# Kernel tuning notes

Hardware: AMD Instinct MI355X
Metric: run time of the kernel (lower is better)

Reference implementation:

```python
import jax, jax.numpy as jnp
import numpy as np

B, PLEN, QLEN, D = 16, 1024, 256, 256
MASK_VALUE = -10000000.0


def setup_inputs() -> dict:
    key = jax.random.key(0)
    k1, k2, k3 = jax.random.split(key, 3)
    passage = jax.random.normal(k1, (B, PLEN, D), dtype=jnp.float32)
    question = jax.random.normal(k2, (B, QLEN, D), dtype=jnp.float32)
    passage_mask = (jnp.arange(PLEN)[None, :] >= int(PLEN * 0.9)).astype(jnp.int32)
    passage_mask = jnp.broadcast_to(passage_mask, (B, PLEN))
    question_mask = (jnp.arange(QLEN)[None, :] >= int(QLEN * 0.9)).astype(jnp.int32)
    question_mask = jnp.broadcast_to(question_mask, (B, QLEN))
    # score_linear: Linear(3d, 1) -> weight vector [3d], scalar bias
    W = jax.random.normal(k3, (3 * D,), dtype=jnp.float32) * 0.05
    b = jnp.zeros((1,), dtype=jnp.float32)
    return {"passage": passage, "question": question,
            "passage_mask": passage_mask, "question_mask": question_mask,
            "W": W, "b": b}


def reference(passage, question, passage_mask, question_mask, W, b):
    d = passage.shape[-1]
    # Decompose Linear([p, q, p*q]) @ W + b into three additive terms --
    # identical math to concat+linear, no [b,plen,qlen,3d] intermediate.
    w_p, w_q, w_pq = W[:d], W[d:2 * d], W[2 * d:]
    score = (jnp.einsum('bpd,d->bp', passage, w_p)[:, :, None]
             + jnp.einsum('bqd,d->bq', question, w_q)[:, None, :]
             + jnp.einsum('bpd,bqd->bpq', passage * w_pq, question)
             + b[0])  # [b, plen, qlen]
    pm = passage_mask.astype(score.dtype)
    qm = question_mask.astype(score.dtype)
    keep = (1.0 - pm)[:, :, None] * (1.0 - qm)[:, None, :]  # [b,plen,qlen]
    mask = 1.0 - keep
    score = score * keep + mask * MASK_VALUE
    p2q_weights = jax.nn.softmax(score, axis=2)
    q2p_weights = jax.nn.softmax(jnp.transpose(score, (0, 2, 1)), axis=2)
    p2q_weights = p2q_weights * keep
    q2p_weights = q2p_weights * jnp.transpose(keep, (0, 2, 1))
    p2q_attention = jnp.einsum('bpq,bqd->bpd', p2q_weights, question)
    q2p_attention = jnp.einsum('bqp,bpd->bqd', q2p_weights, passage)
    coattention = jnp.einsum('bpq,bqd->bpd', p2q_weights, q2p_attention)
    return (p2q_attention, coattention)
```

## Files before the change

### kernel.cpp

```cpp
#include <hip/hip_runtime.h>
#include <math.h>

#define NB 16
#define PLEN 1024
#define QLEN 256
#define DIM 256
#define MASKV -10000000.0f

typedef __attribute__((ext_vector_type(8))) short short8;
typedef __attribute__((ext_vector_type(4))) float f32x4;

union u4x16 { unsigned short u[4]; int2 v; };
union u8x16 { unsigned short u[8]; int4 v; };
union u16x16 { unsigned short u[16]; int4 v[2]; };

__device__ inline unsigned short f2bf(float x) {
  unsigned int u = __float_as_uint(x);
  u += 0x7FFF + ((u >> 16) & 1);
  return (unsigned short)(u >> 16);
}
__device__ inline float bf2f(unsigned short u) {
  return __uint_as_float(((unsigned int)u) << 16);
}
__device__ inline int4 pack8(float4 a, float4 b) {
  u8x16 o;
  o.u[0] = f2bf(a.x); o.u[1] = f2bf(a.y); o.u[2] = f2bf(a.z); o.u[3] = f2bf(a.w);
  o.u[4] = f2bf(b.x); o.u[5] = f2bf(b.y); o.u[6] = f2bf(b.z); o.u[7] = f2bf(b.w);
  return o.v;
}

__global__ __launch_bounds__(1024) void k_scoreA(
    const float* __restrict__ passage, const float* __restrict__ question,
    const float* __restrict__ Wg,
    const int* __restrict__ pmask, const int* __restrict__ qmask,
    const float* __restrict__ bias,
    unsigned short* __restrict__ PbT, unsigned short* __restrict__ QbT,
    float* __restrict__ CM, float* __restrict__ CL,
    float* __restrict__ RM, float* __restrict__ RL,
    unsigned short* __restrict__ P2Q, unsigned short* __restrict__ P2Qt) {
  int bid0 = blockIdx.x;
  int bid = (bid0 & 7) * 32 + (bid0 >> 3);
  int b = bid >> 4;
  int tile = bid & 15;
  int p0 = tile * 64;
  int t = threadIdx.x, lane = t & 63, wv = t >> 6;
  int s = wv >> 2, h = wv & 3;
  __shared__ __align__(16) unsigned short As[2][64][40];
  __shared__ __align__(16) unsigned short Bs[2][256][40];
  __shared__ __align__(16) unsigned short Pl[64][264];
  __shared__ float redM[4][256], redL[4][256];
  __shared__ float rowM[64][4], rowL[64][4];
  __shared__ float spS[64];
  __shared__ float sqS[256];

  int rb = t >> 2, cb = (t & 3) * 8;
  int pr = t >> 4, pc = (t & 15) * 2;
  const float* psrc = passage + ((size_t)b * PLEN + p0 + pr) * DIM;
  const float* qsrc = question + ((size_t)b * QLEN + rb) * DIM;
  const float* wq = Wg + DIM;

  f32x4 acc[4] = {};
  float spp = 0.f, sqq = 0.f;
  float4 qa = *(const float4*)&qsrc[cb];
  float4 qb_ = *(const float4*)&qsrc[cb + 4];
  float2 xv = *(const float2*)(psrc + pc);
  {
    sqq += qa.x * wq[cb]     + qa.y * wq[cb + 1] + qa.z * wq[cb + 2] + qa.w * wq[cb + 3]
         + qb_.x * wq[cb + 4] + qb_.y * wq[cb + 5] + qb_.z * wq[cb + 6] + qb_.w * wq[cb + 7];
    *(int4*)&Bs[0][rb][cb] = pack8(qa, qb_);
    spp += xv.x * Wg[pc] + xv.y * Wg[pc + 1];
    unsigned int raw = (unsigned int)f2bf(xv.x) | (((unsigned int)f2bf(xv.y)) << 16);
    unsigned int wgt = (unsigned int)f2bf(xv.x * Wg[2 * DIM + pc])
                     | (((unsigned int)f2bf(xv.y * Wg[2 * DIM + pc + 1])) << 16);
    *(unsigned int*)&Pl[pr][pc] = raw;
    *(unsigned int*)&As[0][pr][pc] = wgt;
  }
  __syncthreads();
  int cur = 0;
  for (int ki = 0; ki < 8; ++ki) {
    float2 xn; float4 qa2, qb2;
    if (ki < 7) {
      int kt = (ki + 1) * 32;
      qa2 = *(const float4*)&qsrc[kt + cb];
      qb2 = *(const float4*)&qsrc[kt + cb + 4];
      xn = *(const float2*)(psrc + kt + pc);
    }
    short8 af = *(const short8*)&As[cur][s * 16 + (lane & 15)][(lane >> 4) * 8];
    for (int j = 0; j < 4; ++j) {
      short8 bf = *(const short8*)&Bs[cur][h * 64 + j * 16 + (lane & 15)][(lane >> 4) * 8];
      acc[j] = __builtin_amdgcn_mfma_f32_16x16x32_bf16(af, bf, acc[j], 0, 0, 0);
    }
    if (ki < 7) {
      int kt = (ki + 1) * 32;
      int dq = kt + cb, dp = kt + pc;
      sqq += qa2.x * wq[dq]     + qa2.y * wq[dq + 1] + qa2.z * wq[dq + 2] + qa2.w * wq[dq + 3]
           + qb2.x * wq[dq + 4] + qb2.y * wq[dq + 5] + qb2.z * wq[dq + 6] + qb2.w * wq[dq + 7];
      spp += xn.x * Wg[dp] + xn.y * Wg[dp + 1];
      unsigned int raw = (unsigned int)f2bf(xn.x) | (((unsigned int)f2bf(xn.y)) << 16);
      unsigned int wgt = (unsigned int)f2bf(xn.x * Wg[2 * DIM + dp])
                       | (((unsigned int)f2bf(xn.y * Wg[2 * DIM + dp + 1])) << 16);
      int nxt = cur ^ 1;
      *(unsigned int*)&Pl[pr][dp] = raw;
      *(unsigned int*)&As[nxt][pr][pc] = wgt;
      *(int4*)&Bs[nxt][rb][cb] = pack8(qa2, qb2);
      cur = nxt;
    }
    __syncthreads();
  }

  sqq += __shfl_xor(sqq, 1, 64);
  sqq += __shfl_xor(sqq, 2, 64);
  if ((t & 3) == 0) sqS[rb] = sqq;
  spp += __shfl_xor(spp, 1, 64);
  spp += __shfl_xor(spp, 2, 64);
  spp += __shfl_xor(spp, 4, 64);
  spp += __shfl_xor(spp, 8, 64);
  if ((t & 15) == 0) spS[pr] = spp;
  {
    int d = t >> 2, ch = t & 3;
    u16x16 o;
    for (int e = 0; e < 16; ++e) o.u[e] = Pl[ch * 16 + e][d];
    unsigned short* dst = PbT + ((size_t)b * DIM + d) * PLEN + p0 + ch * 16;
    *(int4*)dst = o.v[0];
    *(int4*)(dst + 8) = o.v[1];
  }
  __syncthreads();

  float b0 = bias[0];
  int prow[4]; float spv[4]; int pmv[4];
  for (int r = 0; r < 4; ++r) {
    int rl = s * 16 + (lane >> 4) * 4 + r;
    prow[r] = p0 + rl;
    spv[r] = spS[rl] + b0;
    pmv[r] = pmask[b * PLEN + prow[r]];
  }
  float sqv[4]; int qmv[4];
  for (int j = 0; j < 4; ++j) {
    int q = h * 64 + j * 16 + (lane & 15);
    sqv[j] = sqS[q];
    qmv[j] = qmask[b * QLEN + q];
  }
  for (int j = 0; j < 4; ++j)
    for (int r = 0; r < 4; ++r) {
      float v = acc[j][r] + spv[r] + sqv[j];
      if (pmv[r] | qmv[j]) v = MASKV;
      acc[j][r] = v;
    }

  for (int j = 0; j < 4; ++j) {
    float m = fmaxf(fmaxf(acc[j][0], acc[j][1]), fmaxf(acc[j][2], acc[j][3]));
    m = fmaxf(m, __shfl_xor(m, 16, 64));
    m = fmaxf(m, __shfl_xor(m, 32, 64));
    float e = 0.f;
    for (int r = 0; r < 4; ++r) e += __expf(acc[j][r] - m);
    e += __shfl_xor(e, 16, 64);
    e += __shfl_xor(e, 32, 64);
    if ((lane >> 4) == 0) {
      redM[s][h * 64 + j * 16 + (lane & 15)] = m;
      redL[s][h * 64 + j * 16 + (lane & 15)] = e;
    }
  }
  for (int r = 0; r < 4; ++r) {
    int rl = s * 16 + (lane >> 4) * 4 + r;
    float m = acc[0][r];
    for (int j = 1; j < 4; ++j) m = fmaxf(m, acc[j][r]);
    for (int msk = 1; msk <= 8; msk <<= 1) m = fmaxf(m, __shfl_xor(m, msk, 64));
    float l = 0.f;
    for (int j = 0; j < 4; ++j) l += __expf(acc[j][r] - m);
    for (int msk = 1; msk <= 8; msk <<= 1) l += __shfl_xor(l, msk, 64);
    if ((lane & 15) == 0) { rowM[rl][h] = m; rowL[rl][h] = l; }
  }
  __syncthreads();

  if (t < 256) {
    int q = t;
    float M = fmaxf(fmaxf(redM[0][q], redM[1][q]), fmaxf(redM[2][q], redM[3][q]));
    float L = redL[0][q] * __expf(redM[0][q] - M) + redL[1][q] * __expf(redM[1][q] - M)
            + redL[2][q] * __expf(redM[2][q] - M) + redL[3][q] * __expf(redM[3][q] - M);
    size_t o = ((size_t)b * 16 + tile) * QLEN + q;
    CM[o] = M; CL[o] = L;
  }

  for (int r = 0; r < 4; ++r) {
    int rl = s * 16 + (lane >> 4) * 4 + r;
    float m0 = rowM[rl][0], m1 = rowM[rl][1], m2 = rowM[rl][2], m3 = rowM[rl][3];
    float m = fmaxf(fmaxf(m0, m1), fmaxf(m2, m3));
    float l = rowL[rl][0] * __expf(m0 - m) + rowL[rl][1] * __expf(m1 - m)
            + rowL[rl][2] * __expf(m2 - m) + rowL[rl][3] * __expf(m3 - m);
    if (h == 0 && (lane & 15) == 0) {
      RM[(size_t)b * PLEN + p0 + rl] = m;
      RL[(size_t)b * PLEN + p0 + rl] = l;
    }
    float inv = 1.0f / l;
    for (int j = 0; j < 4; ++j) {
      float e = (pmv[r] | qmv[j]) ? 0.0f : __expf(acc[j][r] - m) * inv;
      Pl[rl][h * 64 + j * 16 + (lane & 15)] = f2bf(e);
    }
  }
  __syncthreads();

  for (int k = 0; k < 2; ++k) {
    int idx = t + k * 1024;
    int row = idx >> 5, c8 = idx & 31;
    *(int4*)&P2Q[((size_t)b * PLEN + p0 + row) * QLEN + c8 * 8] = *(const int4*)&Pl[row][c8 * 8];
  }
  {
    int q = t >> 2, pcc = t & 3;
    u16x16 o;
    for (int e = 0; e < 16; ++e) o.u[e] = Pl[pcc * 16 + e][q];
    unsigned short* dst = P2Qt + ((size_t)b * QLEN + q) * PLEN + p0 + pcc * 16;
    *(int4*)dst = o.v[0];
    *(int4*)(dst + 8) = o.v[1];
  }

  if (tile < 4) {
    __syncthreads();
    int r0 = tile * 64;
    const float* src = question + ((size_t)b * QLEN + r0) * DIM;
    int row = t >> 4, c0 = (t & 15) * 16;
    for (int i = 0; i < 4; ++i) {
      int d = c0 + i * 4;
      float4 x = *(const float4*)&src[(size_t)row * DIM + d];
      u4x16 tv;
      tv.u[0] = f2bf(x.x); tv.u[1] = f2bf(x.y); tv.u[2] = f2bf(x.z); tv.u[3] = f2bf(x.w);
      *(int2*)&Pl[row][d] = tv.v;
    }
    __syncthreads();
    for (int it = 0; it < 2; ++it) {
      int g = t + it * 1024;
      int d = g >> 3, ch = g & 7;
      u8x16 o;
      for (int e = 0; e < 8; ++e) o.u[e] = Pl[ch * 8 + e][d];
      *(int4*)&QbT[(size_t)(b * DIM + d) * QLEN + r0 + ch * 8] = o.v;
    }
  }
}

__global__ __launch_bounds__(512) void k_mid(
    const unsigned short* __restrict__ P2Qt, const unsigned short* __restrict__ PbT,
    const unsigned short* __restrict__ P2Q, const unsigned short* __restrict__ QbT,
    const float* __restrict__ RM, const float* __restrict__ RL,
    const float* __restrict__ CM, const float* __restrict__ CL,
    unsigned short* __restrict__ QATTt, float* __restrict__ out1) {
  __shared__ __align__(16) char smem[40960];
  int t = threadIdx.x, lane = t & 63, wid = t >> 6;

  if (blockIdx.x < NB * 16) {
    int bid = blockIdx.x;
    int b = bid >> 4, dt = (bid >> 2) & 3, qt = bid & 3;
    int wm = wid >> 2, wn = wid & 3;
    typedef unsigned short row72[72];
    row72* Wt = (row72*)smem;
    row72* At = (row72*)(smem + 9216);
    float* MqS = (float*)(smem + 18432);
    float* iLqS = (float*)(smem + 18688);
    if (t < 64) {
      int q = qt * 64 + t;
      float M = CM[((size_t)b * 16) * QLEN + q];
      for (int tm = 1; tm < 16; ++tm)
        M = fmaxf(M, CM[((size_t)b * 16 + tm) * QLEN + q]);
      float L = 0.f;
      for (int tm = 0; tm < 16; ++tm) {
        size_t o = ((size_t)b * 16 + tm) * QLEN + q;
        L += CL[o] * __expf(CM[o] - M);
      }
      MqS[t] = (M < -1.0e6f) ? 1.0e30f : M;
      iLqS[t] = 1.0f / L;
    }
    __syncthreads();

    int rrow = t >> 3;
    int pch = (t & 7) * 8;
    const unsigned short* Wsrc = P2Qt + ((size_t)b * QLEN + qt * 64 + rrow) * PLEN + pch;
    const unsigned short* Asrc = PbT + ((size_t)b * DIM + dt * 64 + rrow) * PLEN + pch;
    const float* rmB = RM + (size_t)b * PLEN + pch;
    const float* rlB = RL + (size_t)b * PLEN + pch;
    float Mq = MqS[rrow], giL = iLqS[rrow];

    f32x4 acc[2] = {};
    int4 wvv = *(const int4*)Wsrc;
    int4 av = *(const int4*)Asrc;
    float4 rm0 = *(const float4*)rmB, rm1 = *(const float4*)(rmB + 4);
    float4 rl0 = *(const float4*)rlB, rl1 = *(const float4*)(rlB + 4);

    for (int ps = 0; ps < 16; ++ps) {
      float rmv[8] = {rm0.x, rm0.y, rm0.z, rm0.w, rm1.x, rm1.y, rm1.z, rm1.w};
      float rlv[8] = {rl0.x, rl0.y, rl0.z, rl0.w, rl1.x, rl1.y, rl1.z, rl1.w};
      const unsigned short* wu = (const unsigned short*)&wvv;
      u8x16 wo;
#pragma unroll
      for (int e = 0; e < 8; ++e) {
        float w = bf2f(wu[e]) * rlv[e] * __expf(rmv[e] - Mq) * giL;
        wo.u[e] = f2bf(w);
      }
      *(int4*)&Wt[rrow][pch] = wo.v;
      *(int4*)&At[rrow][pch] = av;
      if (ps < 15) {
        int off = (ps + 1) * 64;
        wvv = *(const int4*)(Wsrc + off);
        av = *(const int4*)(Asrc + off);
        rm0 = *(const float4*)(rmB + off); rm1 = *(const float4*)(rmB + off + 4);
        rl0 = *(const float4*)(rlB + off); rl1 = *(const float4*)(rlB + off + 4);
      }
      __syncthreads();
      for (int kk = 0; kk < 64; kk += 32) {
        short8 bf = *(const short8*)&Wt[wn * 16 + (lane & 15)][kk + (lane >> 4) * 8];
        for (int i = 0; i < 2; ++i) {
          short8 af = *(const short8*)&At[wm * 32 + i * 16 + (lane & 15)][kk + (lane >> 4) * 8];
          acc[i] = __builtin_amdgcn_mfma_f32_16x16x32_bf16(af, bf, acc[i], 0, 0, 0);
        }
      }
      __syncthreads();
    }
    int d0 = dt * 64 + wm * 32, q0 = qt * 64 + wn * 16;
    for (int i = 0; i < 2; ++i)
      for (int rr = 0; rr < 4; ++rr) {
        int d = d0 + i * 16 + (lane >> 4) * 4 + rr;
        QATTt[((size_t)b * DIM + d) * QLEN + q0 + (lane & 15)] = f2bf(acc[i][rr]);
      }
  } else {
    int bid = blockIdx.x - NB * 16;
    int b = bid >> 4;
    int tm = (bid >> 1) & 7;
    int tn = bid & 1;
    const unsigned short* A  = P2Q + ((size_t)b * PLEN + tm * 128) * QLEN;
    const unsigned short* B1 = QbT + ((size_t)b * DIM + tn * 128) * QLEN;
    typedef unsigned short row40[40];
    row40* As2 = (row40*)smem;
    row40* Bq = (row40*)(smem + 20480);
    int wm = wid >> 2, wn = wid & 3;
    f32x4 acc1[4][2] = {};
    int r = t >> 2, c = (t & 3) * 8;
    int4 rav = *(const int4*)&A[(size_t)r * QLEN + c];
    int4 rb1 = *(const int4*)&B1[(size_t)r * QLEN + c];
    *(int4*)&As2[r][c] = rav;
    *(int4*)&Bq[r][c] = rb1;
    __syncthreads();
    int cur = 0;
    for (int ki = 0; ki < 8; ++ki) {
      if (ki < 7) {
        int kt = (ki + 1) * 32;
        rav = *(const int4*)&A[(size_t)r * QLEN + kt + c];
        rb1 = *(const int4*)&B1[(size_t)r * QLEN + kt + c];
      }
      short8 af[4], b1v[2];
      for (int i = 0; i < 4; ++i)
        af[i] = *(const short8*)&As2[cur * 128 + wm * 64 + i * 16 + (lane & 15)][(lane >> 4) * 8];
      for (int j = 0; j < 2; ++j)
        b1v[j] = *(const short8*)&Bq[cur * 128 + wn * 32 + j * 16 + (lane & 15)][(lane >> 4) * 8];
      for (int i = 0; i < 4; ++i)
        for (int j = 0; j < 2; ++j)
          acc1[i][j] = __builtin_amdgcn_mfma_f32_16x16x32_bf16(af[i], b1v[j], acc1[i][j], 0, 0, 0);
      if (ki < 7) {
        int nxt = cur ^ 1;
        *(int4*)&As2[nxt * 128 + r][c] = rav;
        *(int4*)&Bq[nxt * 128 + r][c] = rb1;
        cur = nxt;
      }
      __syncthreads();
    }
    int p0 = tm * 128 + wm * 64, d0 = tn * 128 + wn * 32;
    for (int i = 0; i < 4; ++i)
      for (int rr = 0; rr < 4; ++rr) {
        int p = p0 + i * 16 + (lane >> 4) * 4 + rr;
        size_t rowo = ((size_t)b * PLEN + p) * DIM;
        for (int j = 0; j < 2; ++j) {
          int d = d0 + j * 16 + (lane & 15);
          out1[rowo + d] = acc1[i][j][rr];
        }
      }
  }
}

__global__ __launch_bounds__(512) void k_final2(
    const unsigned short* __restrict__ P2Q, const unsigned short* __restrict__ QATTt,
    float* __restrict__ out2) {
  int bid = blockIdx.x;
  int b = bid >> 4;
  int tm = (bid >> 1) & 7;
  int tn = bid & 1;
  const unsigned short* A  = P2Q + ((size_t)b * PLEN + tm * 128) * QLEN;
  const unsigned short* B2 = QATTt + ((size_t)b * DIM + tn * 128) * QLEN;
  __shared__ __align__(16) unsigned short As[2][128][40];
  __shared__ __align__(16) unsigned short Bc[2][128][40];
  int t = threadIdx.x, lane = t & 63, wid = t >> 6;
  int wm = wid >> 2, wn = wid & 3;
  f32x4 acc[4][2] = {};
  int r = t >> 2, c = (t & 3) * 8;
  int4 rav = *(const int4*)&A[(size_t)r * QLEN + c];
  int4 rb2 = *(const int4*)&B2[(size_t)r * QLEN + c];
  *(int4*)&As[0][r][c] = rav;
  *(int4*)&Bc[0][r][c] = rb2;
  __syncthreads();
  int cur = 0;
  for (int ki = 0; ki < 8; ++ki) {
    if (ki < 7) {
      int kt = (ki + 1) * 32;
      rav = *(const int4*)&A[(size_t)r * QLEN + kt + c];
      rb2 = *(const int4*)&B2[(size_t)r * QLEN + kt + c];
    }
    short8 af[4], bc[2];
    for (int i = 0; i < 4; ++i)
      af[i] = *(const short8*)&As[cur][wm * 64 + i * 16 + (lane & 15)][(lane >> 4) * 8];
    for (int j = 0; j < 2; ++j)
      bc[j] = *(const short8*)&Bc[cur][wn * 32 + j * 16 + (lane & 15)][(lane >> 4) * 8];
    for (int i = 0; i < 4; ++i)
      for (int j = 0; j < 2; ++j)
        acc[i][j] = __builtin_amdgcn_mfma_f32_16x16x32_bf16(af[i], bc[j], acc[i][j], 0, 0, 0);
    if (ki < 7) {
      int nxt = cur ^ 1;
      *(int4*)&As[nxt][r][c] = rav;
      *(int4*)&Bc[nxt][r][c] = rb2;
      cur = nxt;
    }
    __syncthreads();
  }
  int p0 = tm * 128 + wm * 64, d0 = tn * 128 + wn * 32;
  for (int i = 0; i < 4; ++i)
    for (int rr = 0; rr < 4; ++rr) {
      int p = p0 + i * 16 + (lane >> 4) * 4 + rr;
      size_t rowo = ((size_t)b * PLEN + p) * DIM;
      for (int j = 0; j < 2; ++j) {
        int d = d0 + j * 16 + (lane & 15);
        out2[rowo + d] = acc[i][j][rr];
      }
    }
}

extern "C" void kernel_launch(void* const* d_in, const int* in_sizes, int n_in,
                              void* d_out, int out_size, void* d_ws, size_t ws_size,
                              hipStream_t stream) {
  const float* passage  = (const float*)d_in[0];
  const float* question = (const float*)d_in[1];
  const int*   pmask    = (const int*)d_in[2];
  const int*   qmask    = (const int*)d_in[3];
  const float* W        = (const float*)d_in[4];
  const float* bias     = (const float*)d_in[5];
  float* out = (float*)d_out;

  const size_t NS = (size_t)NB * PLEN * QLEN;
  const size_t NQ = (size_t)NB * QLEN * DIM;
  char* w = (char*)d_ws;
  unsigned short* PbT  = (unsigned short*)w; w += NS * 2;
  unsigned short* QbT  = (unsigned short*)w; w += NQ * 2;
  unsigned short* P2Q  = (unsigned short*)w; w += NS * 2;
  unsigned short* P2Qt = (unsigned short*)w; w += NS * 2;
  unsigned short* QATTt = (unsigned short*)w; w += NQ * 2;
  float* CM = (float*)w;                     w += (size_t)NB * 16 * QLEN * 4;
  float* CL = (float*)w;                     w += (size_t)NB * 16 * QLEN * 4;
  float* RM = (float*)w;                     w += (size_t)NB * PLEN * 4;
  float* RL = (float*)w;

  float* out1 = out;
  float* out2 = out + (size_t)NB * PLEN * DIM;

  k_scoreA<<<dim3(NB * 16), dim3(1024), 0, stream>>>(
      passage, question, W, pmask, qmask, bias, PbT, QbT, CM, CL, RM, RL, P2Q, P2Qt);
  k_mid<<<dim3(NB * 32), dim3(512), 0, stream>>>(
      P2Qt, PbT, P2Q, QbT, RM, RL, CM, CL, QATTt, out1);
  k_final2<<<dim3(NB * 16), dim3(512), 0, stream>>>(
      P2Q, QATTt, out2);
}
```

Measured before the change: 58.62 us.

## Double-buffer k_mid q2p tiles and fold row softmax stats into one scale

The q2p half of k_mid now double-buffers its LDS tiles. The next tile is rescaled and stored while the MFMAs run on the current one, which leaves one barrier per iteration instead of two. The per-row max and sum are folded into a single precomputed scale l*exp(m), and the per-column factor becomes exp(-M)/L. This removes an exp and several loads per element. The combined scale can overflow or underflow fp32 when row maxima are large, which risks numerical error.

```diff
diff --git a/kernel.cpp b/kernel.cpp
--- a/kernel.cpp
+++ b/kernel.cpp
@@ -36,7 +36,7 @@
     const float* __restrict__ bias,
     unsigned short* __restrict__ PbT, unsigned short* __restrict__ QbT,
     float* __restrict__ CM, float* __restrict__ CL,
-    float* __restrict__ RM, float* __restrict__ RL,
+    float* __restrict__ RS,
     unsigned short* __restrict__ P2Q, unsigned short* __restrict__ P2Qt) {
   int bid0 = blockIdx.x;
   int bid = (bid0 & 7) * 32 + (bid0 >> 3);
@@ -187,10 +187,8 @@
     float m = fmaxf(fmaxf(m0, m1), fmaxf(m2, m3));
     float l = rowL[rl][0] * __expf(m0 - m) + rowL[rl][1] * __expf(m1 - m)
             + rowL[rl][2] * __expf(m2 - m) + rowL[rl][3] * __expf(m3 - m);
-    if (h == 0 && (lane & 15) == 0) {
-      RM[(size_t)b * PLEN + p0 + rl] = m;
-      RL[(size_t)b * PLEN + p0 + rl] = l;
-    }
+    if (h == 0 && (lane & 15) == 0)
+      RS[(size_t)b * PLEN + p0 + rl] = l * __expf(m);
     float inv = 1.0f / l;
     for (int j = 0; j < 4; ++j) {
       float e = (pmv[r] | qmv[j]) ? 0.0f : __expf(acc[j][r] - m) * inv;
@@ -239,7 +237,7 @@
 __global__ __launch_bounds__(512) void k_mid(
     const unsigned short* __restrict__ P2Qt, const unsigned short* __restrict__ PbT,
     const unsigned short* __restrict__ P2Q, const unsigned short* __restrict__ QbT,
-    const float* __restrict__ RM, const float* __restrict__ RL,
+    const float* __restrict__ RS,
     const float* __restrict__ CM, const float* __restrict__ CL,
     unsigned short* __restrict__ QATTt, float* __restrict__ out1) {
   __shared__ __align__(16) char smem[40960];
@@ -251,9 +249,8 @@
     int wm = wid >> 2, wn = wid & 3;
     typedef unsigned short row72[72];
     row72* Wt = (row72*)smem;
-    row72* At = (row72*)(smem + 9216);
-    float* MqS = (float*)(smem + 18432);
-    float* iLqS = (float*)(smem + 18688);
+    row72* At = (row72*)(smem + 18432);
+    float* CSs = (float*)(smem + 36864);
     if (t < 64) {
       int q = qt * 64 + t;
       float M = CM[((size_t)b * 16) * QLEN + q];
@@ -264,51 +261,57 @@
         size_t o = ((size_t)b * 16 + tm) * QLEN + q;
         L += CL[o] * __expf(CM[o] - M);
       }
-      MqS[t] = (M < -1.0e6f) ? 1.0e30f : M;
-      iLqS[t] = 1.0f / L;
-    }
-    __syncthreads();
+      CSs[t] = (M < -1.0e6f) ? 0.0f : __expf(-M) / L;
+    }
 
     int rrow = t >> 3;
     int pch = (t & 7) * 8;
     const unsigned short* Wsrc = P2Qt + ((size_t)b * QLEN + qt * 64 + rrow) * PLEN + pch;
     const unsigned short* Asrc = PbT + ((size_t)b * DIM + dt * 64 + rrow) * PLEN + pch;
-    const float* rmB = RM + (size_t)b * PLEN + pch;
-    const float* rlB = RL + (size_t)b * PLEN + pch;
-    float Mq = MqS[rrow], giL = iLqS[rrow];
+    const float* rsB = RS + (size_t)b * PLEN + pch;
 
     f32x4 acc[2] = {};
     int4 wvv = *(const int4*)Wsrc;
     int4 av = *(const int4*)Asrc;
-    float4 rm0 = *(const float4*)rmB, rm1 = *(const float4*)(rmB + 4);
-    float4 rl0 = *(const float4*)rlB, rl1 = *(const float4*)(rlB + 4);
-
-    for (int ps = 0; ps < 16; ++ps) {
-      float rmv[8] = {rm0.x, rm0.y, rm0.z, rm0.w, rm1.x, rm1.y, rm1.z, rm1.w};
-      float rlv[8] = {rl0.x, rl0.y, rl0.z, rl0.w, rl1.x, rl1.y, rl1.z, rl1.w};
+    float4 rs0 = *(const float4*)rsB, rs1 = *(const float4*)(rsB + 4);
+    __syncthreads();
+    float cs = CSs[rrow];
+
+    {
+      float rsv[8] = {rs0.x, rs0.y, rs0.z, rs0.w, rs1.x, rs1.y, rs1.z, rs1.w};
       const unsigned short* wu = (const unsigned short*)&wvv;
       u8x16 wo;
 #pragma unroll
-      for (int e = 0; e < 8; ++e) {
-        float w = bf2f(wu[e]) * rlv[e] * __expf(rmv[e] - Mq) * giL;
-        wo.u[e] = f2bf(w);
-      }
+      for (int e = 0; e < 8; ++e) wo.u[e] = f2bf(bf2f(wu[e]) * rsv[e] * cs);
       *(int4*)&Wt[rrow][pch] = wo.v;
       *(int4*)&At[rrow][pch] = av;
+    }
+    __syncthreads();
+    int cur = 0;
+    for (int ps = 0; ps < 16; ++ps) {
       if (ps < 15) {
         int off = (ps + 1) * 64;
         wvv = *(const int4*)(Wsrc + off);
         av = *(const int4*)(Asrc + off);
-        rm0 = *(const float4*)(rmB + off); rm1 = *(const float4*)(rmB + off + 4);
-        rl0 = *(const float4*)(rlB + off); rl1 = *(const float4*)(rlB + off + 4);
-      }
-      __syncthreads();
+        rs0 = *(const float4*)(rsB + off); rs1 = *(const float4*)(rsB + off + 4);
+      }
       for (int kk = 0; kk < 64; kk += 32) {
-        short8 bf = *(const short8*)&Wt[wn * 16 + (lane & 15)][kk + (lane >> 4) * 8];
+        short8 bf = *(const short8*)&Wt[cur * 64 + wn * 16 + (lane & 15)][kk + (lane >> 4) * 8];
         for (int i = 0; i < 2; ++i) {
-          short8 af = *(const short8*)&At[wm * 32 + i * 16 + (lane & 15)][kk + (lane >> 4) * 8];
+          short8 af = *(const short8*)&At[cur * 64 + wm * 32 + i * 16 + (lane & 15)][kk + (lane >> 4) * 8];
           acc[i] = __builtin_amdgcn_mfma_f32_16x16x32_bf16(af, bf, acc[i], 0, 0, 0);
         }
+      }
+      if (ps < 15) {
+        float rsv[8] = {rs0.x, rs0.y, rs0.z, rs0.w, rs1.x, rs1.y, rs1.z, rs1.w};
+        const unsigned short* wu = (const unsigned short*)&wvv;
+        u8x16 wo;
+#pragma unroll
+        for (int e = 0; e < 8; ++e) wo.u[e] = f2bf(bf2f(wu[e]) * rsv[e] * cs);
+        int nxt = cur ^ 1;
+        *(int4*)&Wt[nxt * 64 + rrow][pch] = wo.v;
+        *(int4*)&At[nxt * 64 + rrow][pch] = av;
+        cur = nxt;
       }
       __syncthreads();
     }
@@ -448,16 +451,15 @@
   unsigned short* QATTt = (unsigned short*)w; w += NQ * 2;
   float* CM = (float*)w;                     w += (size_t)NB * 16 * QLEN * 4;
   float* CL = (float*)w;                     w += (size_t)NB * 16 * QLEN * 4;
-  float* RM = (float*)w;                     w += (size_t)NB * PLEN * 4;
-  float* RL = (float*)w;
+  float* RS = (float*)w;
 
   float* out1 = out;
   float* out2 = out + (size_t)NB * PLEN * DIM;
 
   k_scoreA<<<dim3(NB * 16), dim3(1024), 0, stream>>>(
-      passage, question, W, pmask, qmask, bias, PbT, QbT, CM, CL, RM, RL, P2Q, P2Qt);
+      passage, question, W, pmask, qmask, bias, PbT, QbT, CM, CL, RS, P2Q, P2Qt);
   k_mid<<<dim3(NB * 32), dim3(512), 0, stream>>>(
-      P2Qt, PbT, P2Q, QbT, RM, RL, CM, CL, QATTt, out1);
+      P2Qt, PbT, P2Q, QbT, RS, CM, CL, QATTt, out1);
   k_final2<<<dim3(NB * 16), dim3(512), 0, stream>>>(
       P2Q, QATTt, out2);
 }
```

Measured after the change: 58.78 us. No clear change (+0.3%).
